# Performance work log

Hardware: AMD Instinct MI355X
Metric: run time of the kernel (lower is better)

The kernel has to match this reference:

```python
import jax, jax.numpy as jnp
import numpy as np

NX, NY = 1024, 512
LX, LY = 0.26, 0.12
NU = 1e-4
U_INLET = 0.1
DX = LX / (NX - 1)
DY = LY / (NY - 1)
W_CONT, W_MOM, W_BC = 1.0, 0.1, 1.0


def _pad_x(f):
    # replicate pad along x axis (dim -2)
    return jnp.pad(f, ((0, 0), (0, 0), (1, 1), (0, 0)), mode='edge')


def _pad_y(f):
    return jnp.pad(f, ((0, 0), (0, 0), (0, 0), (1, 1)), mode='edge')


def ddx(f):
    p = _pad_x(f)
    return (p[:, :, 2:, :] - p[:, :, :-2, :]) / (2.0 * DX)


def ddy(f):
    p = _pad_y(f)
    return (p[:, :, :, 2:] - p[:, :, :, :-2]) / (2.0 * DY)


def d2dx2(f):
    p = _pad_x(f)
    return (p[:, :, 2:, :] - 2.0 * f + p[:, :, :-2, :]) / (DX * DX)


def d2dy2(f):
    p = _pad_y(f)
    return (p[:, :, :, 2:] - 2.0 * f + p[:, :, :, :-2]) / (DY * DY)


def masked_mean(x, mask):
    return (x * mask).sum() / jnp.maximum(mask.sum(), 1.0)


def region_masks(x_in):
    r = x_in[:, 1:2].astype(jnp.float32)  # [B,1,NX,NY] region codes
    fluid = (r > 0.5).astype(jnp.float32)
    obstacle = (r < 0.5).astype(jnp.float32)
    wall = ((r > 1.5) & (r < 2.5)).astype(jnp.float32)
    inlet = ((r > 2.5) & (r < 3.5)).astype(jnp.float32)
    outlet = (r > 3.5).astype(jnp.float32)
    noslip = ((obstacle + wall) > 0.5).astype(jnp.float32)
    # interior = fluid with zeroed 1-cell border
    border = jnp.zeros((NX, NY), jnp.float32).at[1:-1, 1:-1].set(1.0)
    interior = fluid * border
    return fluid, interior, noslip, inlet, outlet


def setup_inputs() -> dict:
    key = jax.random.key(0)
    k1, k2 = jax.random.split(key)
    y_hat = jax.random.normal(k1, (16, 3, NX, NY), dtype=jnp.float32)
    x_in = jax.random.randint(k2, (16, 2, NX, NY), 0, 5).astype(jnp.int32)
    return {'y_hat': y_hat, 'x_in': x_in}


def reference(y_hat, x_in):
    ux = y_hat[:, 0:1]
    uy = y_hat[:, 1:2]
    p = y_hat[:, 2:3]
    fluid, interior, noslip, inlet, outlet = region_masks(x_in)

    # continuity
    div = ddx(ux) + ddy(uy)
    l_cont = masked_mean(div ** 2, interior)

    # momentum
    res_x = ux * ddx(ux) + uy * ddy(ux) + ddx(p) - NU * (d2dx2(ux) + d2dy2(ux))
    res_y = ux * ddx(uy) + uy * ddy(uy) + ddy(p) - NU * (d2dx2(uy) + d2dy2(uy))
    l_mom = masked_mean(res_x ** 2, interior) + masked_mean(res_y ** 2, interior)

    # boundary (masked_mean already returns 0 for empty masks via denom clamp)
    l_bc = masked_mean(ux ** 2, noslip) + masked_mean(uy ** 2, noslip)
    l_bc = l_bc + masked_mean((ux - U_INLET) ** 2, inlet) + masked_mean(uy ** 2, inlet)
    l_bc = l_bc + masked_mean(ddx(ux) ** 2, outlet)

    total = W_CONT * l_cont + W_MOM * l_mom + W_BC * l_bc
    return jnp.stack([l_cont, l_mom, l_bc, total])
```

## Files before the change

kernel.cpp:

```cpp
#include <hip/hip_runtime.h>


namespace {
constexpr int NXc   = 1024;
constexpr int NYc   = 512;
constexpr int NXYc  = NXc * NYc;
constexpr int NBc   = 16;
constexpr int NTHR  = 256;
constexpr int NACC  = 10;
constexpr int RROWS = 4;
constexpr int NCHUNK = NXc / RROWS;
constexpr int NWAVE  = NBc * NCHUNK;
constexpr int NBLK   = NWAVE / (NTHR / 64);
}

struct Frow { float4 xl, xh, yl, yh, pl, ph; };

__device__ __forceinline__ Frow ldrow(const float* __restrict__ ux,
                                      const float* __restrict__ uy,
                                      const float* __restrict__ pp, int off) {
  Frow f;
  f.xl = *reinterpret_cast<const float4*>(ux + off);
  f.xh = *reinterpret_cast<const float4*>(ux + off + 4);
  f.yl = *reinterpret_cast<const float4*>(uy + off);
  f.yh = *reinterpret_cast<const float4*>(uy + off + 4);
  f.pl = *reinterpret_cast<const float4*>(pp + off);
  f.ph = *reinterpret_cast<const float4*>(pp + off + 4);
  return f;
}

__global__ __launch_bounds__(NTHR, 2) void pil_main(const float* __restrict__ y,
                                                    const int* __restrict__ xin,
                                                    double* __restrict__ partial) {
  constexpr double DXd = 0.26 / 1023.0;
  constexpr double DYd = 0.12 / 511.0;
  const float INV2DX = (float)(1.0 / (2.0 * DXd));
  const float INV2DY = (float)(1.0 / (2.0 * DYd));
  const float INVDX2 = (float)(1.0 / (DXd * DXd));
  const float INVDY2 = (float)(1.0 / (DYd * DYd));
  constexpr float NU = 1e-4f;
  constexpr float U_INLET = 0.1f;

  const int l     = threadIdx.x & 63;
  const int wv    = (blockIdx.x << 2) | (threadIdx.x >> 6);
  const int chunk = wv & (NCHUNK - 1);
  const int b     = wv >> 8;
  const int i0    = chunk * RROWS;
  const int jc    = l << 3;

  const float* __restrict__ ux = y + (size_t)b * 3 * NXYc;
  const float* __restrict__ uy = ux + NXYc;
  const float* __restrict__ pp = ux + 2 * NXYc;
  const int*   __restrict__ rp = xin + (size_t)(2 * b + 1) * NXYc;

  float a[NACC];
#pragma unroll
  for (int k = 0; k < NACC; ++k) a[k] = 0.f;

  Frow P = ldrow(ux, uy, pp, (i0 > 0 ? i0 - 1 : 0) * NYc + jc);
  Frow C = ldrow(ux, uy, pp, i0 * NYc + jc);
  Frow N = ldrow(ux, uy, pp, (i0 + 1) * NYc + jc);
  int4 rCl = *reinterpret_cast<const int4*>(rp + i0 * NYc + jc);
  int4 rCh = *reinterpret_cast<const int4*>(rp + i0 * NYc + jc + 4);

#pragma unroll
  for (int s = 0; s < RROWS; ++s) {
    const int i = i0 + s;

    Frow F = C;
    int4 rFl = rCl, rFh = rCh;
    if (s < RROWS - 1) {
      F = ldrow(ux, uy, pp, min(i + 2, NXc - 1) * NYc + jc);
      rFl = *reinterpret_cast<const int4*>(rp + (i + 1) * NYc + jc);
      rFh = *reinterpret_cast<const int4*>(rp + (i + 1) * NYc + jc + 4);
    }

    const float cx[8]  = {C.xl.x, C.xl.y, C.xl.z, C.xl.w, C.xh.x, C.xh.y, C.xh.z, C.xh.w};
    const float cy_[8] = {C.yl.x, C.yl.y, C.yl.z, C.yl.w, C.yh.x, C.yh.y, C.yh.z, C.yh.w};
    const float cp_[8] = {C.pl.x, C.pl.y, C.pl.z, C.pl.w, C.ph.x, C.ph.y, C.ph.z, C.ph.w};
    const float pxA[8] = {P.xl.x, P.xl.y, P.xl.z, P.xl.w, P.xh.x, P.xh.y, P.xh.z, P.xh.w};
    const float pyA[8] = {P.yl.x, P.yl.y, P.yl.z, P.yl.w, P.yh.x, P.yh.y, P.yh.z, P.yh.w};
    const float ppA[8] = {P.pl.x, P.pl.y, P.pl.z, P.pl.w, P.ph.x, P.ph.y, P.ph.z, P.ph.w};
    const float nxA[8] = {N.xl.x, N.xl.y, N.xl.z, N.xl.w, N.xh.x, N.xh.y, N.xh.z, N.xh.w};
    const float nyA[8] = {N.yl.x, N.yl.y, N.yl.z, N.yl.w, N.yh.x, N.yh.y, N.yh.z, N.yh.w};
    const float npA[8] = {N.pl.x, N.pl.y, N.pl.z, N.pl.w, N.ph.x, N.ph.y, N.ph.z, N.ph.w};
    const int   rA[8]  = {rCl.x, rCl.y, rCl.z, rCl.w, rCh.x, rCh.y, rCh.z, rCh.w};

    float lxx = __shfl_up(cx[7], 1, 64);    if (l == 0)  lxx = cx[0];
    float rxx = __shfl_down(cx[0], 1, 64);  if (l == 63) rxx = cx[7];
    float lyy = __shfl_up(cy_[7], 1, 64);   if (l == 0)  lyy = cy_[0];
    float ryy = __shfl_down(cy_[0], 1, 64); if (l == 63) ryy = cy_[7];
    float lpp = __shfl_up(cp_[7], 1, 64);   if (l == 0)  lpp = cp_[0];
    float rpp = __shfl_down(cp_[0], 1, 64); if (l == 63) rpp = cp_[7];

    const bool irow = (i >= 1) & (i <= NXc - 2);

#pragma unroll
    for (int e = 0; e < 8; ++e) {
      const int   r    = rA[e];
      const float c_ux = cx[e], c_uy = cy_[e];
      const float uxm = (e == 0) ? lxx : cx[e - 1];
      const float uxp = (e == 7) ? rxx : cx[e + 1];
      const float uym = (e == 0) ? lyy : cy_[e - 1];
      const float uyp = (e == 7) ? ryy : cy_[e + 1];
      const float pm_ = (e == 0) ? lpp : cp_[e - 1];
      const float pq_ = (e == 7) ? rpp : cp_[e + 1];

      const float ddx_ux = (nxA[e] - pxA[e]) * INV2DX;
      const float ddy_ux = (uxp - uxm) * INV2DY;
      const float ddx_uy = (nyA[e] - pyA[e]) * INV2DX;
      const float ddy_uy = (uyp - uym) * INV2DY;

      const bool jedge = ((l == 0) & (e == 0)) | ((l == 63) & (e == 7));
      const bool interior = (r >= 1) & irow & (!jedge);
      if (interior) {
        const float dv    = ddx_ux + ddy_uy;
        const float d2xux = (nxA[e] - 2.f * c_ux + pxA[e]) * INVDX2;
        const float d2yux = (uxp - 2.f * c_ux + uxm) * INVDY2;
        const float d2xuy = (nyA[e] - 2.f * c_uy + pyA[e]) * INVDX2;
        const float d2yuy = (uyp - 2.f * c_uy + uym) * INVDY2;
        const float ddx_p = (npA[e] - ppA[e]) * INV2DX;
        const float ddy_p = (pq_ - pm_) * INV2DY;
        const float rx = c_ux * ddx_ux + c_uy * ddy_ux + ddx_p - NU * (d2xux + d2yux);
        const float ry = c_ux * ddx_uy + c_uy * ddy_uy + ddy_p - NU * (d2xuy + d2yuy);
        a[0] += dv * dv;
        a[1] += rx * rx;
        a[2] += ry * ry;
        a[3] += 1.f;
      }
      if ((r == 0) | (r == 2)) {
        a[4] += c_ux * c_ux + c_uy * c_uy;
        a[5] += 1.f;
      }
      if (r == 3) {
        const float d = c_ux - U_INLET;
        a[6] += d * d + c_uy * c_uy;
        a[7] += 1.f;
      }
      if (r == 4) {
        a[8] += ddx_ux * ddx_ux;
        a[9] += 1.f;
      }
    }

    if (s < RROWS - 1) {
      P = C; C = N; N = F;
      rCl = rFl; rCh = rFh;
    }
  }

#pragma unroll
  for (int k = 0; k < NACC; ++k) {
    float v = a[k];
#pragma unroll
    for (int off = 32; off > 0; off >>= 1) v += __shfl_down(v, off, 64);
    a[k] = v;
  }

  __shared__ double sacc[NTHR / 64][NACC];
  const int lane = threadIdx.x & 63;
  const int wave = threadIdx.x >> 6;
  if (lane == 0) {
#pragma unroll
    for (int k = 0; k < NACC; ++k) sacc[wave][k] = (double)a[k];
  }
  __syncthreads();
  if (threadIdx.x < NACC) {
    double s = 0.0;
#pragma unroll
    for (int w = 0; w < NTHR / 64; ++w) s += sacc[w][threadIdx.x];
    partial[threadIdx.x * NBLK + blockIdx.x] = s;
  }
}

__global__ __launch_bounds__(NTHR) void pil_finalize(const double* __restrict__ partial,
                                                     float* __restrict__ out) {
  __shared__ double sw[NACC][NTHR / 64];
  const int t = threadIdx.x;
  const int lane = t & 63, wave = t >> 6;
#pragma unroll
  for (int k = 0; k < NACC; ++k) {
    double v = 0.0;
    for (int b = t; b < NBLK; b += NTHR) v += partial[k * NBLK + b];
#pragma unroll
    for (int off = 32; off > 0; off >>= 1) v += __shfl_down(v, off, 64);
    if (lane == 0) sw[k][wave] = v;
  }
  __syncthreads();
  if (t == 0) {
    double acc[NACC];
#pragma unroll
    for (int k = 0; k < NACC; ++k) {
      double s = 0.0;
#pragma unroll
      for (int w = 0; w < NTHR / 64; ++w) s += sw[k][w];
      acc[k] = s;
    }
    const double l_cont = acc[0] / fmax(acc[3], 1.0);
    const double l_mom  = (acc[1] + acc[2]) / fmax(acc[3], 1.0);
    const double l_bc   = acc[4] / fmax(acc[5], 1.0)
                        + acc[6] / fmax(acc[7], 1.0)
                        + acc[8] / fmax(acc[9], 1.0);
    const double total  = 1.0 * l_cont + 0.1 * l_mom + 1.0 * l_bc;
    out[0] = (float)l_cont;
    out[1] = (float)l_mom;
    out[2] = (float)l_bc;
    out[3] = (float)total;
  }
}

extern "C" void kernel_launch(void* const* d_in, const int* in_sizes, int n_in,
                              void* d_out, int out_size, void* d_ws, size_t ws_size,
                              hipStream_t stream) {
  const float* y   = (const float*)d_in[0];
  const int*   xin = (const int*)d_in[1];
  double* partial  = (double*)d_ws;

  pil_main<<<NBLK, NTHR, 0, stream>>>(y, xin, partial);
  pil_finalize<<<1, NTHR, 0, stream>>>(partial, (float*)d_out);
}
```

Measured before the change: 49.51 us.

## Process one row per wave with XCD-swizzled block mapping and float partials

```diff
diff --git a/kernel.cpp b/kernel.cpp
--- a/kernel.cpp
+++ b/kernel.cpp
@@ -2,36 +2,21 @@
 
 
 namespace {
-constexpr int NXc   = 1024;
-constexpr int NYc   = 512;
-constexpr int NXYc  = NXc * NYc;
-constexpr int NBc   = 16;
-constexpr int NTHR  = 256;
-constexpr int NACC  = 10;
-constexpr int RROWS = 4;
-constexpr int NCHUNK = NXc / RROWS;
-constexpr int NWAVE  = NBc * NCHUNK;
-constexpr int NBLK   = NWAVE / (NTHR / 64);
-}
-
-struct Frow { float4 xl, xh, yl, yh, pl, ph; };
-
-__device__ __forceinline__ Frow ldrow(const float* __restrict__ ux,
-                                      const float* __restrict__ uy,
-                                      const float* __restrict__ pp, int off) {
-  Frow f;
-  f.xl = *reinterpret_cast<const float4*>(ux + off);
-  f.xh = *reinterpret_cast<const float4*>(ux + off + 4);
-  f.yl = *reinterpret_cast<const float4*>(uy + off);
-  f.yh = *reinterpret_cast<const float4*>(uy + off + 4);
-  f.pl = *reinterpret_cast<const float4*>(pp + off);
-  f.ph = *reinterpret_cast<const float4*>(pp + off + 4);
-  return f;
-}
-
-__global__ __launch_bounds__(NTHR, 2) void pil_main(const float* __restrict__ y,
-                                                    const int* __restrict__ xin,
-                                                    double* __restrict__ partial) {
+constexpr int NXc  = 1024;
+constexpr int NYc  = 512;
+constexpr int NXYc = NXc * NYc;
+constexpr int NBc  = 16;
+constexpr int NTHR = 256;
+constexpr int NACC = 10;
+constexpr int NWAVE = NBc * NXc;
+constexpr int NBLK  = NWAVE / (NTHR / 64);
+constexpr int NXCD  = 8;
+constexpr int QX    = NBLK / NXCD;
+}
+
+__global__ __launch_bounds__(NTHR) void pil_main(const float* __restrict__ y,
+                                                 const int* __restrict__ xin,
+                                                 float* __restrict__ partial) {
   constexpr double DXd = 0.26 / 1023.0;
   constexpr double DYd = 0.12 / 511.0;
   const float INV2DX = (float)(1.0 / (2.0 * DXd));
@@ -41,111 +26,113 @@
   constexpr float NU = 1e-4f;
   constexpr float U_INLET = 0.1f;
 
-  const int l     = threadIdx.x & 63;
-  const int wv    = (blockIdx.x << 2) | (threadIdx.x >> 6);
-  const int chunk = wv & (NCHUNK - 1);
-  const int b     = wv >> 8;
-  const int i0    = chunk * RROWS;
-  const int jc    = l << 3;
+  const int swz = (blockIdx.x % NXCD) * QX + blockIdx.x / NXCD;
+
+  const int l  = threadIdx.x & 63;
+  const int w  = (swz << 2) | (threadIdx.x >> 6);
+  const int i  = w & (NXc - 1);
+  const int b  = w >> 10;
+  const int jc = l << 3;
 
   const float* __restrict__ ux = y + (size_t)b * 3 * NXYc;
   const float* __restrict__ uy = ux + NXYc;
   const float* __restrict__ pp = ux + 2 * NXYc;
   const int*   __restrict__ rp = xin + (size_t)(2 * b + 1) * NXYc;
 
+  const int oc = i * NYc + jc;
+  const int om = (i > 0       ? i - 1 : i) * NYc + jc;
+  const int op = (i < NXc - 1 ? i + 1 : i) * NYc + jc;
+
+  const float4 Pxl = *reinterpret_cast<const float4*>(ux + om);
+  const float4 Pxh = *reinterpret_cast<const float4*>(ux + om + 4);
+  const float4 Pyl = *reinterpret_cast<const float4*>(uy + om);
+  const float4 Pyh = *reinterpret_cast<const float4*>(uy + om + 4);
+  const float4 Ppl = *reinterpret_cast<const float4*>(pp + om);
+  const float4 Pph = *reinterpret_cast<const float4*>(pp + om + 4);
+  const float4 Cxl = *reinterpret_cast<const float4*>(ux + oc);
+  const float4 Cxh = *reinterpret_cast<const float4*>(ux + oc + 4);
+  const float4 Cyl = *reinterpret_cast<const float4*>(uy + oc);
+  const float4 Cyh = *reinterpret_cast<const float4*>(uy + oc + 4);
+  const float4 Cpl = *reinterpret_cast<const float4*>(pp + oc);
+  const float4 Cph = *reinterpret_cast<const float4*>(pp + oc + 4);
+  const float4 Nxl = *reinterpret_cast<const float4*>(ux + op);
+  const float4 Nxh = *reinterpret_cast<const float4*>(ux + op + 4);
+  const float4 Nyl = *reinterpret_cast<const float4*>(uy + op);
+  const float4 Nyh = *reinterpret_cast<const float4*>(uy + op + 4);
+  const float4 Npl = *reinterpret_cast<const float4*>(pp + op);
+  const float4 Nph = *reinterpret_cast<const float4*>(pp + op + 4);
+  const int4  rl   = *reinterpret_cast<const int4*>(rp + oc);
+  const int4  rh   = *reinterpret_cast<const int4*>(rp + oc + 4);
+
   float a[NACC];
 #pragma unroll
   for (int k = 0; k < NACC; ++k) a[k] = 0.f;
 
-  Frow P = ldrow(ux, uy, pp, (i0 > 0 ? i0 - 1 : 0) * NYc + jc);
-  Frow C = ldrow(ux, uy, pp, i0 * NYc + jc);
-  Frow N = ldrow(ux, uy, pp, (i0 + 1) * NYc + jc);
-  int4 rCl = *reinterpret_cast<const int4*>(rp + i0 * NYc + jc);
-  int4 rCh = *reinterpret_cast<const int4*>(rp + i0 * NYc + jc + 4);
-
-#pragma unroll
-  for (int s = 0; s < RROWS; ++s) {
-    const int i = i0 + s;
-
-    Frow F = C;
-    int4 rFl = rCl, rFh = rCh;
-    if (s < RROWS - 1) {
-      F = ldrow(ux, uy, pp, min(i + 2, NXc - 1) * NYc + jc);
-      rFl = *reinterpret_cast<const int4*>(rp + (i + 1) * NYc + jc);
-      rFh = *reinterpret_cast<const int4*>(rp + (i + 1) * NYc + jc + 4);
-    }
-
-    const float cx[8]  = {C.xl.x, C.xl.y, C.xl.z, C.xl.w, C.xh.x, C.xh.y, C.xh.z, C.xh.w};
-    const float cy_[8] = {C.yl.x, C.yl.y, C.yl.z, C.yl.w, C.yh.x, C.yh.y, C.yh.z, C.yh.w};
-    const float cp_[8] = {C.pl.x, C.pl.y, C.pl.z, C.pl.w, C.ph.x, C.ph.y, C.ph.z, C.ph.w};
-    const float pxA[8] = {P.xl.x, P.xl.y, P.xl.z, P.xl.w, P.xh.x, P.xh.y, P.xh.z, P.xh.w};
-    const float pyA[8] = {P.yl.x, P.yl.y, P.yl.z, P.yl.w, P.yh.x, P.yh.y, P.yh.z, P.yh.w};
-    const float ppA[8] = {P.pl.x, P.pl.y, P.pl.z, P.pl.w, P.ph.x, P.ph.y, P.ph.z, P.ph.w};
-    const float nxA[8] = {N.xl.x, N.xl.y, N.xl.z, N.xl.w, N.xh.x, N.xh.y, N.xh.z, N.xh.w};
-    const float nyA[8] = {N.yl.x, N.yl.y, N.yl.z, N.yl.w, N.yh.x, N.yh.y, N.yh.z, N.yh.w};
-    const float npA[8] = {N.pl.x, N.pl.y, N.pl.z, N.pl.w, N.ph.x, N.ph.y, N.ph.z, N.ph.w};
-    const int   rA[8]  = {rCl.x, rCl.y, rCl.z, rCl.w, rCh.x, rCh.y, rCh.z, rCh.w};
-
-    float lxx = __shfl_up(cx[7], 1, 64);    if (l == 0)  lxx = cx[0];
-    float rxx = __shfl_down(cx[0], 1, 64);  if (l == 63) rxx = cx[7];
-    float lyy = __shfl_up(cy_[7], 1, 64);   if (l == 0)  lyy = cy_[0];
-    float ryy = __shfl_down(cy_[0], 1, 64); if (l == 63) ryy = cy_[7];
-    float lpp = __shfl_up(cp_[7], 1, 64);   if (l == 0)  lpp = cp_[0];
-    float rpp = __shfl_down(cp_[0], 1, 64); if (l == 63) rpp = cp_[7];
-
-    const bool irow = (i >= 1) & (i <= NXc - 2);
-
-#pragma unroll
-    for (int e = 0; e < 8; ++e) {
-      const int   r    = rA[e];
-      const float c_ux = cx[e], c_uy = cy_[e];
-      const float uxm = (e == 0) ? lxx : cx[e - 1];
-      const float uxp = (e == 7) ? rxx : cx[e + 1];
-      const float uym = (e == 0) ? lyy : cy_[e - 1];
-      const float uyp = (e == 7) ? ryy : cy_[e + 1];
-      const float pm_ = (e == 0) ? lpp : cp_[e - 1];
-      const float pq_ = (e == 7) ? rpp : cp_[e + 1];
-
-      const float ddx_ux = (nxA[e] - pxA[e]) * INV2DX;
-      const float ddy_ux = (uxp - uxm) * INV2DY;
-      const float ddx_uy = (nyA[e] - pyA[e]) * INV2DX;
-      const float ddy_uy = (uyp - uym) * INV2DY;
-
-      const bool jedge = ((l == 0) & (e == 0)) | ((l == 63) & (e == 7));
-      const bool interior = (r >= 1) & irow & (!jedge);
-      if (interior) {
-        const float dv    = ddx_ux + ddy_uy;
-        const float d2xux = (nxA[e] - 2.f * c_ux + pxA[e]) * INVDX2;
-        const float d2yux = (uxp - 2.f * c_ux + uxm) * INVDY2;
-        const float d2xuy = (nyA[e] - 2.f * c_uy + pyA[e]) * INVDX2;
-        const float d2yuy = (uyp - 2.f * c_uy + uym) * INVDY2;
-        const float ddx_p = (npA[e] - ppA[e]) * INV2DX;
-        const float ddy_p = (pq_ - pm_) * INV2DY;
-        const float rx = c_ux * ddx_ux + c_uy * ddy_ux + ddx_p - NU * (d2xux + d2yux);
-        const float ry = c_ux * ddx_uy + c_uy * ddy_uy + ddy_p - NU * (d2xuy + d2yuy);
-        a[0] += dv * dv;
-        a[1] += rx * rx;
-        a[2] += ry * ry;
-        a[3] += 1.f;
-      }
-      if ((r == 0) | (r == 2)) {
-        a[4] += c_ux * c_ux + c_uy * c_uy;
-        a[5] += 1.f;
-      }
-      if (r == 3) {
-        const float d = c_ux - U_INLET;
-        a[6] += d * d + c_uy * c_uy;
-        a[7] += 1.f;
-      }
-      if (r == 4) {
-        a[8] += ddx_ux * ddx_ux;
-        a[9] += 1.f;
-      }
-    }
-
-    if (s < RROWS - 1) {
-      P = C; C = N; N = F;
-      rCl = rFl; rCh = rFh;
+  const float cx[8]  = {Cxl.x, Cxl.y, Cxl.z, Cxl.w, Cxh.x, Cxh.y, Cxh.z, Cxh.w};
+  const float cy_[8] = {Cyl.x, Cyl.y, Cyl.z, Cyl.w, Cyh.x, Cyh.y, Cyh.z, Cyh.w};
+  const float cp_[8] = {Cpl.x, Cpl.y, Cpl.z, Cpl.w, Cph.x, Cph.y, Cph.z, Cph.w};
+  const float pxA[8] = {Pxl.x, Pxl.y, Pxl.z, Pxl.w, Pxh.x, Pxh.y, Pxh.z, Pxh.w};
+  const float pyA[8] = {Pyl.x, Pyl.y, Pyl.z, Pyl.w, Pyh.x, Pyh.y, Pyh.z, Pyh.w};
+  const float ppA[8] = {Ppl.x, Ppl.y, Ppl.z, Ppl.w, Pph.x, Pph.y, Pph.z, Pph.w};
+  const float nxA[8] = {Nxl.x, Nxl.y, Nxl.z, Nxl.w, Nxh.x, Nxh.y, Nxh.z, Nxh.w};
+  const float nyA[8] = {Nyl.x, Nyl.y, Nyl.z, Nyl.w, Nyh.x, Nyh.y, Nyh.z, Nyh.w};
+  const float npA[8] = {Npl.x, Npl.y, Npl.z, Npl.w, Nph.x, Nph.y, Nph.z, Nph.w};
+  const int   rA[8]  = {rl.x, rl.y, rl.z, rl.w, rh.x, rh.y, rh.z, rh.w};
+
+  float lxx = __shfl_up(cx[7], 1, 64);    if (l == 0)  lxx = cx[0];
+  float rxx = __shfl_down(cx[0], 1, 64);  if (l == 63) rxx = cx[7];
+  float lyy = __shfl_up(cy_[7], 1, 64);   if (l == 0)  lyy = cy_[0];
+  float ryy = __shfl_down(cy_[0], 1, 64); if (l == 63) ryy = cy_[7];
+  float lpp = __shfl_up(cp_[7], 1, 64);   if (l == 0)  lpp = cp_[0];
+  float rpp = __shfl_down(cp_[0], 1, 64); if (l == 63) rpp = cp_[7];
+
+  const bool irow = (i >= 1) & (i <= NXc - 2);
+
+#pragma unroll
+  for (int e = 0; e < 8; ++e) {
+    const int   r    = rA[e];
+    const float c_ux = cx[e], c_uy = cy_[e];
+    const float uxm = (e == 0) ? lxx : cx[e - 1];
+    const float uxp = (e == 7) ? rxx : cx[e + 1];
+    const float uym = (e == 0) ? lyy : cy_[e - 1];
+    const float uyp = (e == 7) ? ryy : cy_[e + 1];
+    const float pm_ = (e == 0) ? lpp : cp_[e - 1];
+    const float pq_ = (e == 7) ? rpp : cp_[e + 1];
+
+    const float ddx_ux = (nxA[e] - pxA[e]) * INV2DX;
+    const float ddy_ux = (uxp - uxm) * INV2DY;
+    const float ddx_uy = (nyA[e] - pyA[e]) * INV2DX;
+    const float ddy_uy = (uyp - uym) * INV2DY;
+
+    const bool jedge = ((l == 0) & (e == 0)) | ((l == 63) & (e == 7));
+    const bool interior = (r >= 1) & irow & (!jedge);
+    if (interior) {
+      const float dv    = ddx_ux + ddy_uy;
+      const float d2xux = (nxA[e] - 2.f * c_ux + pxA[e]) * INVDX2;
+      const float d2yux = (uxp - 2.f * c_ux + uxm) * INVDY2;
+      const float d2xuy = (nyA[e] - 2.f * c_uy + pyA[e]) * INVDX2;
+      const float d2yuy = (uyp - 2.f * c_uy + uym) * INVDY2;
+      const float ddx_p = (npA[e] - ppA[e]) * INV2DX;
+      const float ddy_p = (pq_ - pm_) * INV2DY;
+      const float rx = c_ux * ddx_ux + c_uy * ddy_ux + ddx_p - NU * (d2xux + d2yux);
+      const float ry = c_ux * ddx_uy + c_uy * ddy_uy + ddy_p - NU * (d2xuy + d2yuy);
+      a[0] += dv * dv;
+      a[1] += rx * rx;
+      a[2] += ry * ry;
+      a[3] += 1.f;
+    }
+    if ((r == 0) | (r == 2)) {
+      a[4] += c_ux * c_ux + c_uy * c_uy;
+      a[5] += 1.f;
+    }
+    if (r == 3) {
+      const float d = c_ux - U_INLET;
+      a[6] += d * d + c_uy * c_uy;
+      a[7] += 1.f;
+    }
+    if (r == 4) {
+      a[8] += ddx_ux * ddx_ux;
+      a[9] += 1.f;
     }
   }
 
@@ -157,23 +144,23 @@
     a[k] = v;
   }
 
-  __shared__ double sacc[NTHR / 64][NACC];
+  __shared__ float sacc[NTHR / 64][NACC];
   const int lane = threadIdx.x & 63;
   const int wave = threadIdx.x >> 6;
   if (lane == 0) {
 #pragma unroll
-    for (int k = 0; k < NACC; ++k) sacc[wave][k] = (double)a[k];
+    for (int k = 0; k < NACC; ++k) sacc[wave][k] = a[k];
   }
   __syncthreads();
   if (threadIdx.x < NACC) {
-    double s = 0.0;
-#pragma unroll
-    for (int w = 0; w < NTHR / 64; ++w) s += sacc[w][threadIdx.x];
+    float s = 0.f;
+#pragma unroll
+    for (int ww = 0; ww < NTHR / 64; ++ww) s += sacc[ww][threadIdx.x];
     partial[threadIdx.x * NBLK + blockIdx.x] = s;
   }
 }
 
-__global__ __launch_bounds__(NTHR) void pil_finalize(const double* __restrict__ partial,
+__global__ __launch_bounds__(NTHR) void pil_finalize(const float* __restrict__ partial,
                                                      float* __restrict__ out) {
   __shared__ double sw[NACC][NTHR / 64];
   const int t = threadIdx.x;
@@ -181,7 +168,7 @@
 #pragma unroll
   for (int k = 0; k < NACC; ++k) {
     double v = 0.0;
-    for (int b = t; b < NBLK; b += NTHR) v += partial[k * NBLK + b];
+    for (int b = t; b < NBLK; b += NTHR) v += (double)partial[k * NBLK + b];
 #pragma unroll
     for (int off = 32; off > 0; off >>= 1) v += __shfl_down(v, off, 64);
     if (lane == 0) sw[k][wave] = v;
@@ -214,7 +201,7 @@
                               hipStream_t stream) {
   const float* y   = (const float*)d_in[0];
   const int*   xin = (const int*)d_in[1];
-  double* partial  = (double*)d_ws;
+  float* partial   = (float*)d_ws;
 
   pil_main<<<NBLK, NTHR, 0, stream>>>(y, xin, partial);
   pil_finalize<<<1, NTHR, 0, stream>>>(partial, (float*)d_out);
```

After: 72.29 us. 1.46x slower.
